# Kernel optimization log

Hardware: AMD Instinct MI355X
Metric: run time of the kernel (lower is better)

## Reference

```python
import jax, jax.numpy as jnp
import numpy as np

# --- static config (mirrors init_kwargs / letter_code) ---
BATCH, NODES, AMINO, ATOM = 64, 512, 64, 32
NTYPES = 20
# heavy-atom count minus 1 for the 20 standard amino acids (ARNDCQEGHILKMFPSTWYV)
RES_LENS = np.array([4, 10, 7, 7, 5, 8, 8, 3, 9, 7, 7, 8, 7, 10, 6, 5, 6, 13, 11, 6])
RMAX = int(RES_LENS.max())  # 13


def setup_inputs() -> dict:
    rng = np.random.default_rng(0)
    type_ids = rng.integers(0, NTYPES, size=NODES)           # metadata.seq as type indices
    lens = RES_LENS[type_ids]                                 # residue lengths per node
    valid = np.arange(RMAX)[None, :] < lens[:, None]          # (NODES, RMAX) valid-atom mask
    gather_idx = np.nonzero(valid.reshape(-1))[0]             # flat indices of real atoms

    key = jax.random.key(0)
    k1, k2 = jax.random.split(key)
    x = jax.random.normal(k1, (BATCH, NODES, AMINO, 3), dtype=jnp.float32)
    # stacked per-type TensLinear weights, zero-padded to RMAX residues of output
    W = jax.random.normal(k2, (NTYPES, AMINO, RMAX * ATOM), dtype=jnp.float32) * 0.05
    wmask = (np.arange(RMAX)[None, :, None] < RES_LENS[:, None, None])  # (NTYPES, RMAX, 1)
    wmask = np.broadcast_to(wmask, (NTYPES, RMAX, ATOM)).reshape(NTYPES, 1, RMAX * ATOM)
    W = W * jnp.asarray(wmask, dtype=jnp.float32)
    return {
        "x": x,
        "W": W,
        "type_ids": jnp.asarray(type_ids, dtype=jnp.int64),
        "gather_idx": jnp.asarray(gather_idx, dtype=jnp.int64),
    }


def reference(x, W, type_ids, gather_idx):
    # x: (B, N, amino, 3); W: (T, amino, RMAX*atom); equivariant linear on amino axis
    batch, nodes = x.shape[0], x.shape[1]
    Wg = W[type_ids]                                   # (N, amino, RMAX*atom) type dispatch
    out = jnp.einsum('bnav,naj->bnjv', x, Wg)          # (B, N, RMAX*atom, 3)
    out = out.reshape(batch, nodes * RMAX, ATOM, 3)    # padded per-residue atom blocks
    return out[:, gather_idx]                          # (B, total_atoms, atom, 3) = torch.cat
```

## Files before the change

### kernel.cpp

```cpp
#include <hip/hip_runtime.h>

typedef __bf16 bf16;
typedef __bf16 bf16x8 __attribute__((ext_vector_type(8)));
typedef float f32x4 __attribute__((ext_vector_type(4)));
typedef unsigned short u16;
typedef u16 u16x8 __attribute__((ext_vector_type(8)));
typedef unsigned int u32;

#define BATCH 64
#define NODES 512
#define AMINO 64
#define NTYPES 20
#define RMAX 13
#define NJT 26
#define PADA 72

__constant__ int c_res_lens[NTYPES] = {4,10,7,7,5,8,8,3,9,7,7,8,7,10,6,5,6,13,11,6};

__device__ __forceinline__ u16 f2bf(float f) {
    u32 u; __builtin_memcpy(&u, &f, 4);
    u32 r = u + 0x7FFFu + ((u >> 16) & 1u);
    return (u16)(r >> 16);
}

__device__ __forceinline__ int detect_i64(const int* __restrict__ p) {
    int z = 0;
#pragma unroll
    for (int k = 0; k < 16; ++k) z |= p[2 * k + 1];
    return z == 0;
}
__device__ __forceinline__ int tid_at(const int* __restrict__ p, int n, int is64) {
    return p[is64 ? 2 * n : n];
}

__global__ __launch_bounds__(256) void prep_kernel(const float* __restrict__ W,
                                                   const int* __restrict__ type_ids,
                                                   u16* __restrict__ wswz,
                                                   int* __restrict__ S) {
    if (blockIdx.x < 260) {
        int g = blockIdx.x * 256 + threadIdx.x;
        if (g >= NTYPES * NJT * 2 * 64) return;
        int lane = g & 63;
        int chunk = g >> 6;
        int kh = chunk & 1;
        int tj = chunk >> 1;
        int t = tj / NJT;
        int jt = tj - t * NJT;
        int q = lane >> 4, c = lane & 15;
        int a0 = kh * 32 + q * 8;
        int j = jt * 16 + c;
        u16x8 v;
#pragma unroll
        for (int i = 0; i < 8; ++i)
            v[i] = f2bf(W[(size_t)(t * AMINO + a0 + i) * (RMAX * 32) + j]);
        *(u16x8*)(wswz + (size_t)chunk * 512 + lane * 8) = v;
    } else {
        __shared__ int s[256];
        int is64 = detect_i64(type_ids);
        int i = threadIdx.x;
        int la = c_res_lens[tid_at(type_ids, 2 * i, is64)];
        int lb = c_res_lens[tid_at(type_ids, 2 * i + 1, is64)];
        s[i] = la + lb;
        __syncthreads();
        for (int off = 1; off < 256; off <<= 1) {
            int v = (i >= off) ? s[i - off] : 0;
            __syncthreads();
            s[i] += v;
            __syncthreads();
        }
        int excl = s[i] - (la + lb);
        S[2 * i] = excl;
        S[2 * i + 1] = excl + la;
    }
}

__global__ __launch_bounds__(256) void main_kernel(const float* __restrict__ x,
                                                   const int* __restrict__ type_ids,
                                                   const int* __restrict__ S,
                                                   const u16* __restrict__ wswz,
                                                   float* __restrict__ out,
                                                   int G) {
    __shared__ __align__(16) u16 planes[3][16][PADA];

    const int bid = blockIdx.x;
    const int n = bid >> 2;
    const int m = bid & 3;
    const int tid = threadIdx.x;
    const int w = tid >> 6;
    const int l = tid & 63;

    const int is64 = detect_i64(type_ids);
    const int t = tid_at(type_ids, n, is64);
    const int len = c_res_lens[t];
    const int s0 = S[n];

#pragma unroll
    for (int i = 0; i < 4; ++i) {
        int b16 = i * 4 + w;
        const float* src = x + ((size_t)(m * 16 + b16) * NODES + n) * 192 + l * 3;
        float v0 = src[0];
        float v1 = src[1];
        float v2 = src[2];
        planes[0][b16][l] = f2bf(v0);
        planes[1][b16][l] = f2bf(v1);
        planes[2][b16][l] = f2bf(v2);
    }
    __syncthreads();

    const int q = l >> 4;
    const int c = l & 15;

    union Frag { u16x8 u; bf16x8 b; };
    Frag Af[3][2];
#pragma unroll
    for (int v = 0; v < 3; ++v)
#pragma unroll
        for (int kh = 0; kh < 2; ++kh)
            Af[v][kh].u = *(const u16x8*)(&planes[v][c][kh * 32 + q * 8]);

    for (int r = w; r < len; r += 4) {
        Frag Bf[2][2];
#pragma unroll
        for (int jj = 0; jj < 2; ++jj)
#pragma unroll
            for (int kh = 0; kh < 2; ++kh)
                Bf[jj][kh].u = *(const u16x8*)(wswz +
                                (size_t)((t * NJT + (2 * r + jj)) * 2 + kh) * 512 + l * 8);

        const int g = s0 + r;

        f32x4 acc[2][3];
        const f32x4 z = {0.f, 0.f, 0.f, 0.f};
#pragma unroll
        for (int jj = 0; jj < 2; ++jj)
#pragma unroll
            for (int v = 0; v < 3; ++v) {
                f32x4 a0 = __builtin_amdgcn_mfma_f32_16x16x32_bf16(Af[v][0].b, Bf[jj][0].b, z, 0, 0, 0);
                acc[jj][v] = __builtin_amdgcn_mfma_f32_16x16x32_bf16(Af[v][1].b, Bf[jj][1].b, a0, 0, 0, 0);
            }

#pragma unroll
        for (int reg = 0; reg < 4; ++reg) {
            float* rowp = out + ((size_t)(m * 16 + q * 4 + reg) * G + g) * 96;
#pragma unroll
            for (int jj = 0; jj < 2; ++jj) {
                float* p = rowp + (jj * 16 + c) * 3;
                p[0] = acc[jj][0][reg];
                p[1] = acc[jj][1][reg];
                p[2] = acc[jj][2][reg];
            }
        }
    }
}

extern "C" void kernel_launch(void* const* d_in, const int* in_sizes, int n_in,
                              void* d_out, int out_size, void* d_ws, size_t ws_size,
                              hipStream_t stream) {
    const float* x = (const float*)d_in[0];
    const float* W = (const float*)d_in[1];
    const int* type_ids = (const int*)d_in[2];
    int G = out_size / (BATCH * 32 * 3);

    int* S = (int*)d_ws;
    u16* wswz = (u16*)((char*)d_ws + 4096);

    prep_kernel<<<261, 256, 0, stream>>>(W, type_ids, wswz, S);
    main_kernel<<<NODES * 4, 256, 0, stream>>>(x, type_ids, S, wswz, (float*)d_out, G);
}
```

Before: 129.1 us.

## Fuse prep into main kernel: inline W bf16 conversion and per-block prefix sum

Removes the separate prep kernel. Each block now computes its residue output offset with a wave-level reduction over preceding type ids, and it loads and converts W fp32 to bf16 directly from global memory when building the MFMA B fragments. This drops one kernel launch and the workspace round-trip. In exchange it adds redundant per-block work: up to 512 type-id lookups per wave, and strided scalar fp32 W loads that are repeated across the 2048 blocks instead of one coalesced swizzled load.

Measured after the change: 132.3 us. 2.5% more time.

```diff
diff --git a/kernel.cpp b/kernel.cpp
--- a/kernel.cpp
+++ b/kernel.cpp
@@ -12,7 +12,7 @@
 #define AMINO 64
 #define NTYPES 20
 #define RMAX 13
-#define NJT 26
+#define WCOLS (RMAX * 32)
 #define PADA 72
 
 __constant__ int c_res_lens[NTYPES] = {4,10,7,7,5,8,8,3,9,7,7,8,7,10,6,5,6,13,11,6};
@@ -33,53 +33,11 @@
     return p[is64 ? 2 * n : n];
 }
 
-__global__ __launch_bounds__(256) void prep_kernel(const float* __restrict__ W,
-                                                   const int* __restrict__ type_ids,
-                                                   u16* __restrict__ wswz,
-                                                   int* __restrict__ S) {
-    if (blockIdx.x < 260) {
-        int g = blockIdx.x * 256 + threadIdx.x;
-        if (g >= NTYPES * NJT * 2 * 64) return;
-        int lane = g & 63;
-        int chunk = g >> 6;
-        int kh = chunk & 1;
-        int tj = chunk >> 1;
-        int t = tj / NJT;
-        int jt = tj - t * NJT;
-        int q = lane >> 4, c = lane & 15;
-        int a0 = kh * 32 + q * 8;
-        int j = jt * 16 + c;
-        u16x8 v;
-#pragma unroll
-        for (int i = 0; i < 8; ++i)
-            v[i] = f2bf(W[(size_t)(t * AMINO + a0 + i) * (RMAX * 32) + j]);
-        *(u16x8*)(wswz + (size_t)chunk * 512 + lane * 8) = v;
-    } else {
-        __shared__ int s[256];
-        int is64 = detect_i64(type_ids);
-        int i = threadIdx.x;
-        int la = c_res_lens[tid_at(type_ids, 2 * i, is64)];
-        int lb = c_res_lens[tid_at(type_ids, 2 * i + 1, is64)];
-        s[i] = la + lb;
-        __syncthreads();
-        for (int off = 1; off < 256; off <<= 1) {
-            int v = (i >= off) ? s[i - off] : 0;
-            __syncthreads();
-            s[i] += v;
-            __syncthreads();
-        }
-        int excl = s[i] - (la + lb);
-        S[2 * i] = excl;
-        S[2 * i + 1] = excl + la;
-    }
-}
-
-__global__ __launch_bounds__(256) void main_kernel(const float* __restrict__ x,
-                                                   const int* __restrict__ type_ids,
-                                                   const int* __restrict__ S,
-                                                   const u16* __restrict__ wswz,
-                                                   float* __restrict__ out,
-                                                   int G) {
+__global__ __launch_bounds__(256) void fused_kernel(const float* __restrict__ x,
+                                                    const float* __restrict__ W,
+                                                    const int* __restrict__ type_ids,
+                                                    float* __restrict__ out,
+                                                    int G) {
     __shared__ __align__(16) u16 planes[3][16][PADA];
 
     const int bid = blockIdx.x;
@@ -92,7 +50,6 @@
     const int is64 = detect_i64(type_ids);
     const int t = tid_at(type_ids, n, is64);
     const int len = c_res_lens[t];
-    const int s0 = S[n];
 
 #pragma unroll
     for (int i = 0; i < 4; ++i) {
@@ -105,6 +62,13 @@
         planes[1][b16][l] = f2bf(v1);
         planes[2][b16][l] = f2bf(v2);
     }
+
+    int part = 0;
+    for (int k = l; k < n; k += 64) part += c_res_lens[tid_at(type_ids, k, is64)];
+#pragma unroll
+    for (int off = 1; off < 64; off <<= 1) part += __shfl_xor(part, off);
+    const int s0 = part;
+
     __syncthreads();
 
     const int q = l >> 4;
@@ -118,14 +82,20 @@
         for (int kh = 0; kh < 2; ++kh)
             Af[v][kh].u = *(const u16x8*)(&planes[v][c][kh * 32 + q * 8]);
 
+    const float* Wqc = W + (size_t)(t * AMINO + q * 8) * WCOLS + c;
+
     for (int r = w; r < len; r += 4) {
         Frag Bf[2][2];
 #pragma unroll
         for (int jj = 0; jj < 2; ++jj)
 #pragma unroll
-            for (int kh = 0; kh < 2; ++kh)
-                Bf[jj][kh].u = *(const u16x8*)(wswz +
-                                (size_t)((t * NJT + (2 * r + jj)) * 2 + kh) * 512 + l * 8);
+            for (int kh = 0; kh < 2; ++kh) {
+                const float* p = Wqc + kh * 32 * WCOLS + r * 32 + jj * 16;
+                u16x8 v;
+#pragma unroll
+                for (int i = 0; i < 8; ++i) v[i] = f2bf(p[i * WCOLS]);
+                Bf[jj][kh].u = v;
+            }
 
         const int g = s0 + r;
 
@@ -144,10 +114,10 @@
             float* rowp = out + ((size_t)(m * 16 + q * 4 + reg) * G + g) * 96;
 #pragma unroll
             for (int jj = 0; jj < 2; ++jj) {
-                float* p = rowp + (jj * 16 + c) * 3;
-                p[0] = acc[jj][0][reg];
-                p[1] = acc[jj][1][reg];
-                p[2] = acc[jj][2][reg];
+                float* p2 = rowp + (jj * 16 + c) * 3;
+                p2[0] = acc[jj][0][reg];
+                p2[1] = acc[jj][1][reg];
+                p2[2] = acc[jj][2][reg];
             }
         }
     }
@@ -161,9 +131,5 @@
     const int* type_ids = (const int*)d_in[2];
     int G = out_size / (BATCH * 32 * 3);
 
-    int* S = (int*)d_ws;
-    u16* wswz = (u16*)((char*)d_ws + 4096);
-
-    prep_kernel<<<261, 256, 0, stream>>>(W, type_ids, wswz, S);
-    main_kernel<<<NODES * 4, 256, 0, stream>>>(x, type_ids, S, wswz, (float*)d_out, G);
+    fused_kernel<<<NODES * 4, 256, 0, stream>>>(x, W, type_ids, (float*)d_out, G);
 }
```
